# Performance work log

Hardware: AMD Instinct MI355X
Metric: run time of the kernel (lower is better)

The kernel has to match this reference:

```python
import jax, jax.numpy as jnp
import numpy as np

N = 32768   # atoms/nodes
E = 4       # chemical elements
C = 128     # input channels per irrep
K = 128     # output channels per irrep
LMAX = 3    # 4 l-blocks -> 16 lm rows


def setup_inputs() -> dict:
    key = jax.random.key(0)
    kx, ky, kw = jax.random.split(key, 3)
    x = jax.random.normal(kx, (N, (LMAX + 1) ** 2, C), dtype=jnp.float32)
    # one-hot element encoding per node
    elem = jax.random.randint(ky, (N,), 0, E)
    y = jax.nn.one_hot(elem, E, dtype=jnp.float32)
    # per-element, per-l weight blocks [E, 4, C, K]
    weights = jax.random.normal(kw, (E, LMAX + 1, C, K), dtype=jnp.float32)
    return {"x": x, "y": y, "weights": weights}


def reference(x, y, weights):
    # x: [N, 16, C]  y: [N, E] one-hot  weights: [E, 4, C, K]
    n, _, c = x.shape
    e, nl, _, k = weights.shape
    path_weight = 1.0 / jnp.sqrt(jnp.asarray(c, x.dtype))  # e3nn uvw normalization
    outs = []
    for l in range(nl):
        s = l * l
        m = 2 * l + 1
        xb = x[:, s:s + m, :]                      # [N, 2l+1, C]
        acc = jnp.zeros((n, m, k), x.dtype)
        for el in range(e):
            # mask-weighted grouped GEMM: only nodes of element `el` contribute
            acc = acc + y[:, el, None, None] * jnp.einsum('nmc,ck->nmk', xb, weights[el, l])
        outs.append(acc * path_weight)
    return jnp.concatenate(outs, axis=1)           # [N, 16, K]
```

## Files before the change

### kernel.cpp

```cpp
#include <hip/hip_runtime.h>

#define NS 32768
#define NE 4

typedef __attribute__((ext_vector_type(4))) float f32x4;
typedef __attribute__((ext_vector_type(8))) short bf16x8;

__device__ __forceinline__ unsigned short f2bf(float f) {
    unsigned int u = __float_as_uint(f);
    u = (u + 0x7fffu + ((u >> 16) & 1u)) >> 16;
    return (unsigned short)u;
}

__device__ __forceinline__ int expert_of(const float4 yr) {
    int e = 0;
    if (yr.y > 0.5f) e = 1;
    else if (yr.z > 0.5f) e = 2;
    else if (yr.w > 0.5f) e = 3;
    return e;
}

__global__ void prep_count(const float* __restrict__ W,
                           unsigned short* __restrict__ Wt,
                           const float* __restrict__ y,
                           int* __restrict__ bcnt) {
    const int b = blockIdx.x;
    if (b < 16) {
        const float* w = W + (size_t)b * 16384;
        unsigned short* wt = Wt + (size_t)b * 16384;
        for (int i = threadIdx.x; i < 16384; i += 256) {
            int c = i & 127, k = i >> 7;
            wt[k * 128 + c] = f2bf(w[c * 128 + k]);
        }
        return;
    }
    __shared__ int c[4][4];
    const int blk = b - 16;
    int n = blk * 256 + threadIdx.x;
    int e = expert_of(((const float4*)y)[n]);
    const int lane = threadIdx.x & 63;
    const int wv = threadIdx.x >> 6;
#pragma unroll
    for (int ee = 0; ee < NE; ++ee) {
        unsigned long long m = __ballot(e == ee);
        if (lane == 0) c[wv][ee] = __popcll(m);
    }
    __syncthreads();
    if (threadIdx.x < 4)
        bcnt[threadIdx.x * 128 + blk] = c[0][threadIdx.x] + c[1][threadIdx.x] +
                                        c[2][threadIdx.x] + c[3][threadIdx.x];
}

__global__ void prep_fill(const float* __restrict__ y,
                          const int* __restrict__ bcnt, int* __restrict__ idx,
                          int* __restrict__ cnt) {
    __shared__ int sh_boff[4];
    __shared__ int wcnt[4][4];
    const int blk = blockIdx.x;
    const int lane = threadIdx.x & 63;
    const int wv = threadIdx.x >> 6;

    {
        int c0 = bcnt[wv * 128 + lane];
        int c1 = bcnt[wv * 128 + 64 + lane];
        int part = ((lane < blk) ? c0 : 0) + ((lane + 64 < blk) ? c1 : 0);
        int tot = c0 + c1;
#pragma unroll
        for (int d = 1; d < 64; d <<= 1) {
            part += __shfl_xor(part, d);
            tot += __shfl_xor(tot, d);
        }
        if (lane == 0) {
            sh_boff[wv] = part;
            if (blk == 0) cnt[wv] = tot;
        }
    }

    int n = blk * 256 + threadIdx.x;
    int e = expert_of(((const float4*)y)[n]);
    int rank = 0;
#pragma unroll
    for (int ee = 0; ee < NE; ++ee) {
        unsigned long long m = __ballot(e == ee);
        if (lane == 0) wcnt[wv][ee] = __popcll(m);
        if (e == ee) rank = __popcll(m & ((1ull << lane) - 1ull));
    }
    __syncthreads();
#pragma unroll
    for (int w = 0; w < 4; ++w)
        if (w < wv) rank += wcnt[w][e];
    idx[e * NS + sh_boff[e] + rank] = n;
}

template <int L, int M>
__device__ __forceinline__ void gemm_body(
    int e, int bi, int nb, unsigned char* lds, const float* __restrict__ x,
    const unsigned short* __restrict__ Wt, const int* __restrict__ cnt,
    const int* __restrict__ idx, float* __restrict__ out) {
    const int rows_total = cnt[e] * M;

    {
        const unsigned char* wp =
            (const unsigned char*)(Wt + (size_t)(e * 4 + L) * 16384);
        const int t = threadIdx.x;
#pragma unroll
        for (int q = 0; q < 4; ++q) {
            int o = q * 8192 + t * 16;
            uint4 v = *(const uint4*)(wp + o);
            int so = o ^ (((o >> 8) & 7) << 4);
            *(uint4*)(lds + so) = v;
        }
    }
    __syncthreads();

    const int lane = threadIdx.x & 63;
    const int wv = threadIdx.x >> 6;
    const int li = lane & 15;
    const int half = lane >> 4;
    const int i5 = lane >> 5;
    const int c32 = lane & 31;
    const int* idxe = idx + e * NS;
    unsigned char* xl = lds + 32768 + wv * 4096;

    for (int tile = bi; tile * 128 < rows_total; tile += nb) {
        const int gbase = tile * 128 + wv * 16;

        int g = gbase + li;
        bool valid = g < rows_total;
        int gc = valid ? g : rows_total - 1;
        int pos = gc / M;
        int jj = gc - pos * M;
        int xrow = idxe[pos] * 16 + L * L + jj;

        f32x4 bv[8];
#pragma unroll
        for (int q = 0; q < 8; ++q) {
            int gt = gbase + 2 * q + i5;
            int gtc = gt < rows_total ? gt : rows_total - 1;
            int p = gtc / M;
            int jq = gtc - p * M;
            int nr = idxe[p] * 16 + L * L + jq;
            bv[q] = *(const f32x4*)(x + (size_t)nr * 128 + c32 * 4);
        }
#pragma unroll
        for (int q = 0; q < 8; ++q) {
            int tr = 2 * q + i5;
            unsigned int p0 = (unsigned int)f2bf(bv[q].x) |
                              ((unsigned int)f2bf(bv[q].y) << 16);
            unsigned int p1 = (unsigned int)f2bf(bv[q].z) |
                              ((unsigned int)f2bf(bv[q].w) << 16);
            uint2 pk; pk.x = p0; pk.y = p1;
            int off = (c32 * 8) ^ ((tr & 7) << 4);
            *(uint2*)(xl + tr * 256 + off) = pk;
        }

        f32x4 acc[8];
#pragma unroll
        for (int t = 0; t < 8; ++t) acc[t] = (f32x4){0.f, 0.f, 0.f, 0.f};

#pragma unroll
        for (int kk = 0; kk < 4; ++kk) {
            int co = (kk * 64 + half * 16) ^ ((li & 7) << 4);
            bf16x8 bfrag = *(const bf16x8*)(xl + li * 256 + co);
#pragma unroll
            for (int t = 0; t < 8; ++t) {
                bf16x8 afrag = *(const bf16x8*)(lds + (t * 16 + li) * 256 + co);
                acc[t] = __builtin_amdgcn_mfma_f32_16x16x32_bf16(afrag, bfrag,
                                                                 acc[t], 0, 0, 0);
            }
        }

        if (valid) {
            float* orow = out + (size_t)xrow * 128;
            const float pw = 0.088388347648318447f;
#pragma unroll
            for (int t = 0; t < 8; ++t) {
                *(f32x4*)(orow + t * 16 + half * 4) = acc[t] * pw;
            }
        }
    }
}

__global__ __launch_bounds__(512, 2) void gemm_main(
    const float* __restrict__ x, const unsigned short* __restrict__ Wt,
    const int* __restrict__ cnt, const int* __restrict__ idx,
    float* __restrict__ out) {
    __shared__ __align__(16) unsigned char lds[65536];
    const int b = blockIdx.x;
    const int e = b >> 8;
    const int r = b & 255;
    if (r < 16)       gemm_body<0, 1>(e, r,       16,  lds, x, Wt, cnt, idx, out);
    else if (r < 64)  gemm_body<1, 3>(e, r - 16,  48,  lds, x, Wt, cnt, idx, out);
    else if (r < 144) gemm_body<2, 5>(e, r - 64,  80,  lds, x, Wt, cnt, idx, out);
    else              gemm_body<3, 7>(e, r - 144, 112, lds, x, Wt, cnt, idx, out);
}

extern "C" void kernel_launch(void* const* d_in, const int* in_sizes, int n_in,
                              void* d_out, int out_size, void* d_ws,
                              size_t ws_size, hipStream_t stream) {
    const float* x = (const float*)d_in[0];
    const float* y = (const float*)d_in[1];
    const float* W = (const float*)d_in[2];
    float* out = (float*)d_out;

    char* ws = (char*)d_ws;
    int* cnt = (int*)ws;
    int* idx = (int*)(ws + 64);
    unsigned short* Wt = (unsigned short*)(ws + 64 + NE * NS * 4);
    int* bcnt = (int*)(ws + 64 + NE * NS * 4 + 16 * 16384 * 2);

    prep_count<<<16 + 128, 256, 0, stream>>>(W, Wt, y, bcnt);
    prep_fill<<<128, 256, 0, stream>>>(y, bcnt, idx, cnt);
    gemm_main<<<1024, 512, 0, stream>>>(x, Wt, cnt, idx, out);
}
```

Measured before the change: 134.7 us.

## Pair l-blocks per workgroup with node-tiled work split across waves

The GEMM kernel is restructured so each 256-thread workgroup handles a fixed chunk of 64 nodes and holds two weight panels in LDS (l=0 with l=3, or l=1 with l=2). This balances the rows per workgroup, since 1+7 and 3+5 rows per node each total 8. The grid changes from 1024 persistent strided blocks to 4096 node-chunk blocks that exit early when they fall past an element's count. In exchange it uses more LDS per block (80 KB), which may reduce occupancy, and weight panels are reloaded more often across the many small blocks.

```diff
diff --git a/kernel.cpp b/kernel.cpp
--- a/kernel.cpp
+++ b/kernel.cpp
@@ -59,7 +59,6 @@
     const int blk = blockIdx.x;
     const int lane = threadIdx.x & 63;
     const int wv = threadIdx.x >> 6;
-
     {
         int c0 = bcnt[wv * 128 + lane];
         int c1 = bcnt[wv * 128 + 64 + lane];
@@ -75,7 +74,6 @@
             if (blk == 0) cnt[wv] = tot;
         }
     }
-
     int n = blk * 256 + threadIdx.x;
     int e = expert_of(((const float4*)y)[n]);
     int rank = 0;
@@ -93,85 +91,62 @@
 }
 
 template <int L, int M>
-__device__ __forceinline__ void gemm_body(
-    int e, int bi, int nb, unsigned char* lds, const float* __restrict__ x,
-    const unsigned short* __restrict__ Wt, const int* __restrict__ cnt,
-    const int* __restrict__ idx, float* __restrict__ out) {
-    const int rows_total = cnt[e] * M;
-
-    {
-        const unsigned char* wp =
-            (const unsigned char*)(Wt + (size_t)(e * 4 + L) * 16384);
-        const int t = threadIdx.x;
-#pragma unroll
-        for (int q = 0; q < 4; ++q) {
-            int o = q * 8192 + t * 16;
-            uint4 v = *(const uint4*)(wp + o);
-            int so = o ^ (((o >> 8) & 7) << 4);
-            *(uint4*)(lds + so) = v;
-        }
-    }
-    __syncthreads();
-
+__device__ __forceinline__ void sub_tile(
+    int s_l, int tile, int cnt_e, const int* __restrict__ idxe,
+    const float* __restrict__ x, const unsigned char* __restrict__ wpan,
+    unsigned char* __restrict__ xl, float* __restrict__ out) {
     const int lane = threadIdx.x & 63;
-    const int wv = threadIdx.x >> 6;
     const int li = lane & 15;
     const int half = lane >> 4;
     const int i5 = lane >> 5;
     const int c32 = lane & 31;
-    const int* idxe = idx + e * NS;
-    unsigned char* xl = lds + 32768 + wv * 4096;
-
-    for (int tile = bi; tile * 128 < rows_total; tile += nb) {
-        const int gbase = tile * 128 + wv * 16;
-
-        int g = gbase + li;
-        bool valid = g < rows_total;
-        int gc = valid ? g : rows_total - 1;
-        int pos = gc / M;
-        int jj = gc - pos * M;
-        int xrow = idxe[pos] * 16 + L * L + jj;
-
-        f32x4 bv[8];
-#pragma unroll
-        for (int q = 0; q < 8; ++q) {
-            int gt = gbase + 2 * q + i5;
-            int gtc = gt < rows_total ? gt : rows_total - 1;
-            int p = gtc / M;
-            int jq = gtc - p * M;
-            int nr = idxe[p] * 16 + L * L + jq;
-            bv[q] = *(const f32x4*)(x + (size_t)nr * 128 + c32 * 4);
-        }
-#pragma unroll
-        for (int q = 0; q < 8; ++q) {
-            int tr = 2 * q + i5;
-            unsigned int p0 = (unsigned int)f2bf(bv[q].x) |
-                              ((unsigned int)f2bf(bv[q].y) << 16);
-            unsigned int p1 = (unsigned int)f2bf(bv[q].z) |
-                              ((unsigned int)f2bf(bv[q].w) << 16);
-            uint2 pk; pk.x = p0; pk.y = p1;
-            int off = (c32 * 8) ^ ((tr & 7) << 4);
-            *(uint2*)(xl + tr * 256 + off) = pk;
-        }
-
-        f32x4 acc[8];
-#pragma unroll
-        for (int t = 0; t < 8; ++t) acc[t] = (f32x4){0.f, 0.f, 0.f, 0.f};
-
-#pragma unroll
-        for (int kk = 0; kk < 4; ++kk) {
-            int co = (kk * 64 + half * 16) ^ ((li & 7) << 4);
-            bf16x8 bfrag = *(const bf16x8*)(xl + li * 256 + co);
-#pragma unroll
-            for (int t = 0; t < 8; ++t) {
-                bf16x8 afrag = *(const bf16x8*)(lds + (t * 16 + li) * 256 + co);
-                acc[t] = __builtin_amdgcn_mfma_f32_16x16x32_bf16(afrag, bfrag,
-                                                                 acc[t], 0, 0, 0);
-            }
-        }
-
-        if (valid) {
-            float* orow = out + (size_t)xrow * 128;
+
+    f32x4 bv[8];
+#pragma unroll
+    for (int p = 0; p < 8; ++p) {
+        int r = s_l * 16 + 2 * p + i5;
+        int q = r / M;
+        int j = r - q * M;
+        int pos = tile * 16 + q;
+        int pc = pos < cnt_e ? pos : cnt_e - 1;
+        int row = idxe[pc] * 16 + L * L + j;
+        bv[p] = *(const f32x4*)(x + (size_t)row * 128 + c32 * 4);
+    }
+#pragma unroll
+    for (int p = 0; p < 8; ++p) {
+        int tr = 2 * p + i5;
+        unsigned int p0 = (unsigned int)f2bf(bv[p].x) |
+                          ((unsigned int)f2bf(bv[p].y) << 16);
+        unsigned int p1 = (unsigned int)f2bf(bv[p].z) |
+                          ((unsigned int)f2bf(bv[p].w) << 16);
+        uint2 pk; pk.x = p0; pk.y = p1;
+        int off = (c32 * 8) ^ ((tr & 7) << 4);
+        *(uint2*)(xl + tr * 256 + off) = pk;
+    }
+
+    f32x4 acc[8];
+#pragma unroll
+    for (int t = 0; t < 8; ++t) acc[t] = (f32x4){0.f, 0.f, 0.f, 0.f};
+
+#pragma unroll
+    for (int kk = 0; kk < 4; ++kk) {
+        int co = (kk * 64 + half * 16) ^ ((li & 7) << 4);
+        bf16x8 bfrag = *(const bf16x8*)(xl + li * 256 + co);
+#pragma unroll
+        for (int t = 0; t < 8; ++t) {
+            bf16x8 afrag = *(const bf16x8*)(wpan + (t * 16 + li) * 256 + co);
+            acc[t] = __builtin_amdgcn_mfma_f32_16x16x32_bf16(afrag, bfrag,
+                                                             acc[t], 0, 0, 0);
+        }
+    }
+
+    {
+        int r = s_l * 16 + li;
+        int q = r / M;
+        int j = r - q * M;
+        int pos = tile * 16 + q;
+        if (pos < cnt_e) {
+            float* orow = out + (size_t)(idxe[pos] * 16 + L * L + j) * 128;
             const float pw = 0.088388347648318447f;
 #pragma unroll
             for (int t = 0; t < 8; ++t) {
@@ -181,18 +156,62 @@
     }
 }
 
-__global__ __launch_bounds__(512, 2) void gemm_main(
+__global__ __launch_bounds__(256, 2) void gemm_main(
     const float* __restrict__ x, const unsigned short* __restrict__ Wt,
     const int* __restrict__ cnt, const int* __restrict__ idx,
     float* __restrict__ out) {
-    __shared__ __align__(16) unsigned char lds[65536];
+    __shared__ __align__(16) unsigned char lds[81920];
     const int b = blockIdx.x;
-    const int e = b >> 8;
-    const int r = b & 255;
-    if (r < 16)       gemm_body<0, 1>(e, r,       16,  lds, x, Wt, cnt, idx, out);
-    else if (r < 64)  gemm_body<1, 3>(e, r - 16,  48,  lds, x, Wt, cnt, idx, out);
-    else if (r < 144) gemm_body<2, 5>(e, r - 64,  80,  lds, x, Wt, cnt, idx, out);
-    else              gemm_body<3, 7>(e, r - 144, 112, lds, x, Wt, cnt, idx, out);
+    const int e = b >> 10;
+    const int rem = b & 1023;
+    const int pair = rem & 1;
+    const int u = rem >> 1;
+    const int cnt_e = cnt[e];
+    if (u * 64 >= cnt_e) return;
+
+    {
+        const unsigned char* pa =
+            (const unsigned char*)(Wt + (size_t)(e * 4 + (pair ? 1 : 0)) * 16384);
+        const unsigned char* pb =
+            (const unsigned char*)(Wt + (size_t)(e * 4 + (pair ? 2 : 3)) * 16384);
+        const int t = threadIdx.x;
+#pragma unroll
+        for (int qq = 0; qq < 8; ++qq) {
+            int o = qq * 4096 + t * 16;
+            uint4 va = *(const uint4*)(pa + o);
+            uint4 vb = *(const uint4*)(pb + o);
+            int so = o ^ (((o >> 8) & 7) << 4);
+            *(uint4*)(lds + so) = va;
+            *(uint4*)(lds + 32768 + so) = vb;
+        }
+    }
+    __syncthreads();
+
+    const int wv = threadIdx.x >> 6;
+    const int* idxe = idx + e * NS;
+    unsigned char* xl = lds + 65536 + wv * 4096;
+
+    for (int tt = 0; tt < 4; ++tt) {
+        int tile = u * 4 + tt;
+        if (tile * 16 >= cnt_e) break;
+        if (pair == 0) {
+            if (wv == 0) {
+                sub_tile<0, 1>(0, tile, cnt_e, idxe, x, lds, xl, out);
+                sub_tile<3, 7>(3, tile, cnt_e, idxe, x, lds + 32768, xl, out);
+            } else {
+                sub_tile<3, 7>(wv - 1, tile, cnt_e, idxe, x, lds + 32768, xl, out);
+                sub_tile<3, 7>(wv + 3, tile, cnt_e, idxe, x, lds + 32768, xl, out);
+            }
+        } else {
+            if (wv < 3) {
+                sub_tile<1, 3>(wv, tile, cnt_e, idxe, x, lds, xl, out);
+                sub_tile<2, 5>(wv + 1, tile, cnt_e, idxe, x, lds + 32768, xl, out);
+            } else {
+                sub_tile<2, 5>(0, tile, cnt_e, idxe, x, lds + 32768, xl, out);
+                sub_tile<2, 5>(4, tile, cnt_e, idxe, x, lds + 32768, xl, out);
+            }
+        }
+    }
 }
 
 extern "C" void kernel_launch(void* const* d_in, const int* in_sizes, int n_in,
@@ -211,5 +230,5 @@
 
     prep_count<<<16 + 128, 256, 0, stream>>>(W, Wt, y, bcnt);
     prep_fill<<<128, 256, 0, stream>>>(y, bcnt, idx, cnt);
-    gemm_main<<<1024, 512, 0, stream>>>(x, Wt, cnt, idx, out);
-}
+    gemm_main<<<4096, 256, 0, stream>>>(x, Wt, cnt, idx, out);
+}
```

New measurement: 251.2 us. +86.5%, slower.
